# Performance work log

Measured on AMD Instinct MI355X. Metric: run time of the kernel, lower is better.

## Reference

```python
import jax, jax.numpy as jnp
import numpy as np

D_IN = 300      # mol2vec feature dim
H = 64          # neurons[0] == neurons[1]


def _l2norm(x):
    # F.normalize(x, p=2, dim=-1)
    n = jnp.sqrt(jnp.sum(x * x, axis=-1, keepdims=True))
    return x / jnp.maximum(n, 1e-12)


def _scatter_mean(x, row, col, n_nodes):
    # scatter_mean(x[col], row, dim_size=n_nodes); empty rows -> 0
    s = jax.ops.segment_sum(x[col], row, num_segments=n_nodes)
    c = jax.ops.segment_sum(jnp.ones((row.shape[0], 1), x.dtype), row, num_segments=n_nodes)
    return s / jnp.maximum(c, 1.0)


def _sage_base(x, edges, W, b, n_nodes):
    agg = _scatter_mean(x, edges[0], edges[1], n_nodes)
    h = jnp.concatenate([agg, x], axis=1) @ W + b
    return _l2norm(h)


def _sage_deep(x1, x2, pos_e, neg_e, W, b, n_nodes):
    a1 = _scatter_mean(x1, pos_e[0], pos_e[1], n_nodes)
    a2 = _scatter_mean(x2, neg_e[0], neg_e[1], n_nodes)
    h = jnp.concatenate([a1, a2, x1], axis=1) @ W + b
    return _l2norm(h)


def setup_inputs() -> dict:
    key = jax.random.key(0)
    ks = jax.random.split(key, 16)
    N, E = 8192, 262144

    X = jax.random.normal(ks[0], (N, D_IN), dtype=jnp.float32)

    def make_edges(k):
        e = jax.random.randint(k, (2, E), 0, N, dtype=jnp.int64)
        # no self loops (module calls remove_self_loops)
        col = jnp.where(e[1] == e[0], (e[1] + 1) % N, e[1])
        return jnp.stack([e[0], col])

    positive_edges = make_edges(ks[1])
    negative_edges = make_edges(ks[2])

    labels = jax.random.normal(ks[3], (N * N,), dtype=jnp.float32)
    label_mask = jax.random.uniform(ks[4], (N, N), dtype=jnp.float32)

    sd = lambda fan_in: 1.0 / np.sqrt(fan_in)
    W_pos_base = jax.random.normal(ks[5], (2 * D_IN, H), dtype=jnp.float32) * sd(2 * D_IN)
    b_pos_base = jnp.zeros((H,), dtype=jnp.float32)
    W_neg_base = jax.random.normal(ks[6], (2 * D_IN, H), dtype=jnp.float32) * sd(2 * D_IN)
    b_neg_base = jnp.zeros((H,), dtype=jnp.float32)
    W_pos_deep = jax.random.normal(ks[7], (3 * H, H), dtype=jnp.float32) * sd(3 * H)
    b_pos_deep = jnp.zeros((H,), dtype=jnp.float32)
    W_neg_deep = jax.random.normal(ks[8], (3 * H, H), dtype=jnp.float32) * sd(3 * H)
    b_neg_deep = jnp.zeros((H,), dtype=jnp.float32)

    return {
        "X": X, "positive_edges": positive_edges, "negative_edges": negative_edges,
        "labels": labels, "label_mask": label_mask,
        "W_pos_base": W_pos_base, "b_pos_base": b_pos_base,
        "W_neg_base": W_neg_base, "b_neg_base": b_neg_base,
        "W_pos_deep": W_pos_deep, "b_pos_deep": b_pos_deep,
        "W_neg_deep": W_neg_deep, "b_neg_deep": b_neg_deep,
    }


def reference(X, positive_edges, negative_edges, labels, label_mask,
              W_pos_base, b_pos_base, W_neg_base, b_neg_base,
              W_pos_deep, b_pos_deep, W_neg_deep, b_neg_deep):
    N = X.shape[0]
    h_pos = jnp.tanh(_sage_base(X, positive_edges, W_pos_base, b_pos_base, N))
    h_neg = jnp.tanh(_sage_base(X, negative_edges, W_neg_base, b_neg_base, N))
    h_pos2 = jnp.tanh(_sage_deep(h_pos, h_neg, positive_edges, negative_edges, W_pos_deep, b_pos_deep, N))
    h_neg2 = jnp.tanh(_sage_deep(h_neg, h_pos, positive_edges, negative_edges, W_neg_deep, b_neg_deep, N))
    z = jnp.concatenate([h_pos2, h_neg2], axis=1)           # [N, 2H]
    X_mol = _l2norm(z)
    pred = ((X_mol @ X_mol.T) * label_mask).reshape(-1)      # [N*N]
    loss = jnp.mean((pred - labels) ** 2)
    return (loss, X_mol, pred)
```

## Files before the change

### kernel.cpp

```cpp
#include <hip/hip_runtime.h>
#include <hip/hip_bf16.h>

#define DIN 300
#define KP  320
#define NH  64

typedef __bf16 bf16x8 __attribute__((ext_vector_type(8)));
typedef float  f32x4  __attribute__((ext_vector_type(4)));

__device__ inline float wave_sum(float v){
#pragma unroll
  for (int m = 32; m >= 1; m >>= 1) v += __shfl_xor(v, m, 64);
  return v;
}

__global__ __launch_bounds__(256) void k_prep(const float* __restrict__ X,
                                              __hip_bfloat16* __restrict__ Xb,
                                              const float* __restrict__ Wpb,
                                              const float* __restrict__ Wnb,
                                              __hip_bfloat16* __restrict__ Wtb,
                                              const int* __restrict__ pr, const int* __restrict__ nr,
                                              int* __restrict__ cp, int* __restrict__ cn,
                                              int E, int N){
  int b = blockIdx.x;
  if (b < N){
    const float* xr = X + (size_t)b * DIN;
    __hip_bfloat16* o = Xb + (size_t)b * KP;
    for (int k = threadIdx.x; k < KP; k += 256)
      o[k] = __float2bfloat16(k < DIN ? xr[k] : 0.f);
  } else if (b < N + 256){
    int c = b - N;
    int sel = c >> 6, jj = c & 63;
    const float* W = (sel < 2 ? Wpb : Wnb) + (size_t)(sel & 1) * DIN * NH + jj;
    __hip_bfloat16* o = Wtb + (size_t)c * KP;
    for (int k = threadIdx.x; k < KP; k += 256)
      o[k] = __float2bfloat16(k < DIN ? W[(size_t)k * NH] : 0.f);
  } else {
    int i = (b - N - 256) * 256 + threadIdx.x;
    if (i < E){ atomicAdd(cp + pr[i], 1); atomicAdd(cn + nr[i], 1); }
  }
}

__global__ __launch_bounds__(256) void k_gemm_base(const __hip_bfloat16* __restrict__ Xb,
                                                   const __hip_bfloat16* __restrict__ Wtb,
                                                   float* __restrict__ XW){
  const int wave = threadIdx.x >> 6, lane = threadIdx.x & 63;
  const int ti = blockIdx.y * 64 + wave * 16;
  const int cj = blockIdx.x * 64;
  const int r0 = lane & 15, kq = (lane >> 4) * 8;
  const unsigned short* Xp = (const unsigned short*)Xb;
  const unsigned short* Wp = (const unsigned short*)Wtb;
  f32x4 acc[4] = {};
  for (int ks = 0; ks < KP / 32; ++ks){
    int kb = ks * 32 + kq;
    bf16x8 a = *(const bf16x8*)(Xp + (size_t)(ti + r0) * KP + kb);
#pragma unroll
    for (int js = 0; js < 4; ++js){
      bf16x8 b = *(const bf16x8*)(Wp + (size_t)(cj + js * 16 + r0) * KP + kb);
      acc[js] = __builtin_amdgcn_mfma_f32_16x16x32_bf16(a, b, acc[js], 0, 0, 0);
    }
  }
  const int orow = ti + (lane >> 4) * 4;
  const int oc = cj + (lane & 15);
#pragma unroll
  for (int js = 0; js < 4; ++js)
#pragma unroll
    for (int i = 0; i < 4; ++i)
      XW[(size_t)(orow + i) * 256 + oc + js * 16] = acc[js][i];
}

__global__ __launch_bounds__(1024) void k_scan(const int* __restrict__ c0, int* __restrict__ o0,
                                               const int* __restrict__ c1, int* __restrict__ o1, int n){
  const int* cnt = blockIdx.x ? c1 : c0;
  int* off = blockIdx.x ? o1 : o0;
  __shared__ int lds[1024];
  int t = threadIdx.x;
  int ept = n >> 10;
  int s = 0;
  for (int i = 0; i < ept; ++i) s += cnt[t * ept + i];
  lds[t] = s; __syncthreads();
  for (int d = 1; d < 1024; d <<= 1){
    int add = (t >= d) ? lds[t - d] : 0;
    __syncthreads();
    lds[t] += add;
    __syncthreads();
  }
  int base = t ? lds[t - 1] : 0;
  for (int i = 0; i < ept; ++i){ off[t * ept + i] = base; base += cnt[t * ept + i]; }
}

__global__ void k_fill(const int* __restrict__ pr, const int* __restrict__ pc,
                       const int* __restrict__ nr, const int* __restrict__ nc,
                       const int* __restrict__ op, const int* __restrict__ on,
                       int* __restrict__ curp, int* __restrict__ curn,
                       int* __restrict__ adjp, int* __restrict__ adjn, int E){
  int i = blockIdx.x * 256 + threadIdx.x;
  if (i < E){
    int r = pr[i]; int p = atomicAdd(curp + r, 1); adjp[op[r] + p] = pc[i];
    r = nr[i];     p = atomicAdd(curn + r, 1);     adjn[on[r] + p] = nc[i];
  }
}

__device__ inline float gather_mean(const float* __restrict__ XW, const int* __restrict__ adj,
                                    int base, int d, int col){
  float s = 0.f; int j = 0;
  for (; j + 4 <= d; j += 4){
    int n0 = adj[base + j], n1 = adj[base + j + 1], n2 = adj[base + j + 2], n3 = adj[base + j + 3];
    s += XW[(size_t)n0 * 256 + col] + XW[(size_t)n1 * 256 + col]
       + XW[(size_t)n2 * 256 + col] + XW[(size_t)n3 * 256 + col];
  }
  for (; j < d; ++j) s += XW[(size_t)adj[base + j] * 256 + col];
  return s / (float)(d > 0 ? d : 1);
}

__global__ __launch_bounds__(256) void k_base(const float* __restrict__ XW,
    const int* __restrict__ adjp, const int* __restrict__ offp, const int* __restrict__ cntp,
    const int* __restrict__ adjn, const int* __restrict__ offn, const int* __restrict__ cntn,
    const float* __restrict__ bp, const float* __restrict__ bn,
    float* __restrict__ hp, float* __restrict__ hn){
  const int wave = threadIdx.x >> 6, lane = threadIdx.x & 63;
  const int node = blockIdx.x * 4 + wave;
  {
    float s = gather_mean(XW, adjp, offp[node], cntp[node], lane);
    float pre = s + XW[(size_t)node * 256 + 64 + lane] + bp[lane];
    float nrm = sqrtf(wave_sum(pre * pre));
    hp[(size_t)node * 64 + lane] = tanhf(pre / fmaxf(nrm, 1e-12f));
  }
  {
    float s = gather_mean(XW, adjn, offn[node], cntn[node], lane + 128);
    float pre = s + XW[(size_t)node * 256 + 192 + lane] + bn[lane];
    float nrm = sqrtf(wave_sum(pre * pre));
    hn[(size_t)node * 64 + lane] = tanhf(pre / fmaxf(nrm, 1e-12f));
  }
}

__global__ __launch_bounds__(256) void k_deep(const float* __restrict__ hp, const float* __restrict__ hn,
    const int* __restrict__ adjp, const int* __restrict__ offp, const int* __restrict__ cntp,
    const int* __restrict__ adjn, const int* __restrict__ offn, const int* __restrict__ cntn,
    const float* __restrict__ Wpd, const float* __restrict__ bpd,
    const float* __restrict__ Wnd, const float* __restrict__ bnd,
    float* __restrict__ xmol, __hip_bfloat16* __restrict__ Xmb){
  const int wave = threadIdx.x >> 6, lane = threadIdx.x & 63;
  const int node = blockIdx.x * 4 + wave;
  const float mhp = hp[(size_t)node * 64 + lane];
  const float mhn = hn[(size_t)node * 64 + lane];
  float a1p = 0.f, a1n = 0.f;
  {
    int d = cntp[node], base = offp[node]; int j = 0;
    for (; j + 2 <= d; j += 2){
      int n0 = adjp[base + j], n1 = adjp[base + j + 1];
      a1p += hp[(size_t)n0 * 64 + lane] + hp[(size_t)n1 * 64 + lane];
      a1n += hn[(size_t)n0 * 64 + lane] + hn[(size_t)n1 * 64 + lane];
    }
    for (; j < d; ++j){ int n0 = adjp[base + j]; a1p += hp[(size_t)n0 * 64 + lane]; a1n += hn[(size_t)n0 * 64 + lane]; }
    float inv = 1.f / (float)(d > 0 ? d : 1); a1p *= inv; a1n *= inv;
  }
  float a2p = 0.f, a2n = 0.f;
  {
    int d = cntn[node], base = offn[node]; int j = 0;
    for (; j + 2 <= d; j += 2){
      int n0 = adjn[base + j], n1 = adjn[base + j + 1];
      a2p += hn[(size_t)n0 * 64 + lane] + hn[(size_t)n1 * 64 + lane];
      a2n += hp[(size_t)n0 * 64 + lane] + hp[(size_t)n1 * 64 + lane];
    }
    for (; j < d; ++j){ int n0 = adjn[base + j]; a2p += hn[(size_t)n0 * 64 + lane]; a2n += hp[(size_t)n0 * 64 + lane]; }
    float inv = 1.f / (float)(d > 0 ? d : 1); a2p *= inv; a2n *= inv;
  }
  float accp = bpd[lane], accn = bnd[lane];
#pragma unroll 4
  for (int k = 0; k < 64; ++k){
    float p1 = __shfl(a1p, k, 64), p2 = __shfl(a2p, k, 64), p3 = __shfl(mhp, k, 64);
    float q1 = __shfl(a1n, k, 64), q2 = __shfl(a2n, k, 64), q3 = __shfl(mhn, k, 64);
    accp += p1 * Wpd[k * 64 + lane] + p2 * Wpd[(64 + k) * 64 + lane] + p3 * Wpd[(128 + k) * 64 + lane];
    accn += q1 * Wnd[k * 64 + lane] + q2 * Wnd[(64 + k) * 64 + lane] + q3 * Wnd[(128 + k) * 64 + lane];
  }
  float np = sqrtf(wave_sum(accp * accp));
  float h2p = tanhf(accp / fmaxf(np, 1e-12f));
  float nn = sqrtf(wave_sum(accn * accn));
  float h2n = tanhf(accn / fmaxf(nn, 1e-12f));
  float nz = sqrtf(wave_sum(h2p * h2p + h2n * h2n));
  float xp = h2p / fmaxf(nz, 1e-12f);
  float xn = h2n / fmaxf(nz, 1e-12f);
  xmol[(size_t)node * 128 + lane] = xp;
  xmol[(size_t)node * 128 + 64 + lane] = xn;
  Xmb[(size_t)node * 128 + lane] = __float2bfloat16(xp);
  Xmb[(size_t)node * 128 + 64 + lane] = __float2bfloat16(xn);
}

__global__ __launch_bounds__(256, 3) void k_pred(const __hip_bfloat16* __restrict__ Xmb,
    const float* __restrict__ mask, const float* __restrict__ labels,
    float* __restrict__ pred, float* __restrict__ partial, int N){
  const int wave = threadIdx.x >> 6, lane = threadIdx.x & 63;
  const int ti = blockIdx.y * 64 + wave * 16;
  const int tj = blockIdx.x * 128;
  const int r0 = lane & 15, kq = (lane >> 4) * 8;
  const unsigned short* X = (const unsigned short*)Xmb;
  f32x4 acc[2][4] = {};
#pragma unroll
  for (int ks = 0; ks < 4; ++ks){
    int kb = ks * 32 + kq;
    bf16x8 a = *(const bf16x8*)(X + (size_t)(ti + r0) * 128 + kb);
#pragma unroll
    for (int pan = 0; pan < 2; ++pan)
#pragma unroll
      for (int js = 0; js < 4; ++js){
        bf16x8 b = *(const bf16x8*)(X + (size_t)(tj + pan * 64 + js * 16 + r0) * 128 + kb);
        acc[pan][js] = __builtin_amdgcn_mfma_f32_16x16x32_bf16(a, b, acc[pan][js], 0, 0, 0);
      }
  }
  const int hi = lane >> 5, c = lane & 31;
  f32x4 m[8], lb[8];
#pragma unroll
  for (int g = 0; g < 8; ++g){
    size_t idx = (size_t)(ti + g * 2 + hi) * N + tj + c * 4;
    m[g]  = __builtin_nontemporal_load((const f32x4*)(mask + idx));
    lb[g] = __builtin_nontemporal_load((const f32x4*)(labels + idx));
  }
#pragma unroll
  for (int g = 0; g < 8; ++g)
    asm volatile("" : "+v"(m[g]), "+v"(lb[g]));
  __shared__ float tile[4][16][132];
  __shared__ float wsum[4];
  const int rb = (lane >> 4) * 4, c16 = lane & 15;
#pragma unroll
  for (int pan = 0; pan < 2; ++pan)
#pragma unroll
    for (int js = 0; js < 4; ++js)
#pragma unroll
      for (int i = 0; i < 4; ++i)
        tile[wave][rb + i][pan * 64 + js * 16 + c16] = acc[pan][js][i];
  float lsum = 0.f;
#pragma unroll
  for (int g = 0; g < 8; ++g){
    int row = g * 2 + hi;
    f32x4 a = *(const f32x4*)&tile[wave][row][c * 4];
    f32x4 pv = a * m[g];
    f32x4 d = pv - lb[g];
    lsum += d[0]*d[0] + d[1]*d[1] + d[2]*d[2] + d[3]*d[3];
    size_t idx = (size_t)(ti + row) * N + tj + c * 4;
    __builtin_nontemporal_store(pv[0], pred + idx);
    __builtin_nontemporal_store(pv[1], pred + idx + 1);
    __builtin_nontemporal_store(pv[2], pred + idx + 2);
    __builtin_nontemporal_store(pv[3], pred + idx + 3);
  }
  lsum = wave_sum(lsum);
  if (lane == 0) wsum[wave] = lsum;
  __syncthreads();
  if (threadIdx.x == 0)
    partial[blockIdx.y * gridDim.x + blockIdx.x] = wsum[0] + wsum[1] + wsum[2] + wsum[3];
}

__global__ __launch_bounds__(1024) void k_loss_fin(const float* __restrict__ partial,
                                                   float* __restrict__ out, float inv, int n){
  float s = 0.f;
  for (int i = threadIdx.x; i < n; i += 1024) s += partial[i];
  s = wave_sum(s);
  __shared__ float ws[16];
  if ((threadIdx.x & 63) == 0) ws[threadIdx.x >> 6] = s;
  __syncthreads();
  if (threadIdx.x == 0){
    float t = 0.f;
#pragma unroll
    for (int w = 0; w < 16; ++w) t += ws[w];
    out[0] = t * inv;
  }
}

extern "C" void kernel_launch(void* const* d_in, const int* in_sizes, int n_in,
                              void* d_out, int out_size, void* d_ws, size_t ws_size,
                              hipStream_t stream){
  const float* X      = (const float*)d_in[0];
  const int*   pe     = (const int*)d_in[1];
  const int*   ne     = (const int*)d_in[2];
  const float* labels = (const float*)d_in[3];
  const float* mask   = (const float*)d_in[4];
  const float* Wpb    = (const float*)d_in[5];
  const float* bpb    = (const float*)d_in[6];
  const float* Wnb    = (const float*)d_in[7];
  const float* bnb    = (const float*)d_in[8];
  const float* Wpd    = (const float*)d_in[9];
  const float* bpd    = (const float*)d_in[10];
  const float* Wnd    = (const float*)d_in[11];
  const float* bnd    = (const float*)d_in[12];
  const int N = in_sizes[0] / DIN;
  const int E = in_sizes[1] / 2;

  char* ws = (char*)d_ws;
  size_t off = 0;
  auto alloc = [&](size_t bytes){ void* p = ws + off; off = (off + bytes + 255) & ~(size_t)255; return p; };
  float* XW            = (float*)alloc((size_t)N * 256 * 4);
  float* hp            = (float*)alloc((size_t)N * 64 * 4);
  float* hn            = (float*)alloc((size_t)N * 64 * 4);
  __hip_bfloat16* Xmb  = (__hip_bfloat16*)alloc((size_t)N * 128 * 2);
  __hip_bfloat16* Xb   = (__hip_bfloat16*)alloc((size_t)N * KP * 2);
  __hip_bfloat16* Wtb  = (__hip_bfloat16*)alloc((size_t)256 * KP * 2);
  int* adjp            = (int*)alloc((size_t)E * 4);
  int* adjn            = (int*)alloc((size_t)E * 4);
  char* zbase = ws + off;
  int* cntp            = (int*)alloc((size_t)N * 4);
  int* cntn            = (int*)alloc((size_t)N * 4);
  int* curp            = (int*)alloc((size_t)N * 4);
  int* curn            = (int*)alloc((size_t)N * 4);
  size_t zbytes = (size_t)((ws + off) - zbase);
  int* offp            = (int*)alloc((size_t)N * 4);
  int* offn            = (int*)alloc((size_t)N * 4);
  float* partial       = (float*)alloc((size_t)(N / 64) * (N / 128) * 4);
  (void)ws_size; (void)n_in; (void)out_size;

  float* out_loss = (float*)d_out;
  float* out_xmol = out_loss + 1;
  float* out_pred = out_xmol + (size_t)N * 128;

  hipMemsetAsync(zbase, 0, zbytes, stream);
  k_prep<<<N + 256 + (E + 255) / 256, 256, 0, stream>>>(X, Xb, Wpb, Wnb, Wtb,
                                                        pe, ne, cntp, cntn, E, N);
  k_gemm_base<<<dim3(4, N / 64), 256, 0, stream>>>(Xb, Wtb, XW);
  k_scan<<<2, 1024, 0, stream>>>(cntp, offp, cntn, offn, N);
  k_fill<<<(E + 255) / 256, 256, 0, stream>>>(pe, pe + E, ne, ne + E, offp, offn, curp, curn, adjp, adjn, E);
  k_base<<<N / 4, 256, 0, stream>>>(XW, adjp, offp, cntp, adjn, offn, cntn, bpb, bnb, hp, hn);
  k_deep<<<N / 4, 256, 0, stream>>>(hp, hn, adjp, offp, cntp, adjn, offn, cntn,
                                    Wpd, bpd, Wnd, bnd, out_xmol, Xmb);
  k_pred<<<dim3(N / 128, N / 64), 256, 0, stream>>>(Xmb, mask, labels, out_pred, partial, N);
  k_loss_fin<<<1, 1024, 0, stream>>>(partial, out_loss, 1.0f / ((float)N * (float)N), (N / 64) * (N / 128));
}
```

Measured before the change: 367.9 us.

## Vectorize X bf16 conversion, widen gather unrolls, relax k_pred launch bounds

```diff
diff --git a/kernel.cpp b/kernel.cpp
--- a/kernel.cpp
+++ b/kernel.cpp
@@ -7,6 +7,7 @@
 
 typedef __bf16 bf16x8 __attribute__((ext_vector_type(8)));
 typedef float  f32x4  __attribute__((ext_vector_type(4)));
+typedef short  s16x4  __attribute__((ext_vector_type(4)));
 
 __device__ inline float wave_sum(float v){
 #pragma unroll
@@ -25,9 +26,21 @@
   int b = blockIdx.x;
   if (b < N){
     const float* xr = X + (size_t)b * DIN;
-    __hip_bfloat16* o = Xb + (size_t)b * KP;
-    for (int k = threadIdx.x; k < KP; k += 256)
-      o[k] = __float2bfloat16(k < DIN ? xr[k] : 0.f);
+    unsigned short* o = (unsigned short*)(Xb + (size_t)b * KP);
+    int k = threadIdx.x;
+    if (k < 80){
+      s16x4 v;
+      if (k < 75){
+        f32x4 x = *(const f32x4*)(xr + k * 4);
+#pragma unroll
+        for (int j = 0; j < 4; ++j){
+          union { float f; unsigned u; } cv; cv.f = x[j];
+          unsigned r = (cv.u + 0x7FFF + ((cv.u >> 16) & 1)) >> 16;
+          v[j] = (short)r;
+        }
+      } else v = (s16x4){0,0,0,0};
+      *(s16x4*)(o + k * 4) = v;
+    }
   } else if (b < N + 256){
     int c = b - N;
     int sel = c >> 6, jj = c & 63;
@@ -103,13 +116,18 @@
 
 __device__ inline float gather_mean(const float* __restrict__ XW, const int* __restrict__ adj,
                                     int base, int d, int col){
-  float s = 0.f; int j = 0;
-  for (; j + 4 <= d; j += 4){
-    int n0 = adj[base + j], n1 = adj[base + j + 1], n2 = adj[base + j + 2], n3 = adj[base + j + 3];
-    s += XW[(size_t)n0 * 256 + col] + XW[(size_t)n1 * 256 + col]
-       + XW[(size_t)n2 * 256 + col] + XW[(size_t)n3 * 256 + col];
-  }
-  for (; j < d; ++j) s += XW[(size_t)adj[base + j] * 256 + col];
+  float s0 = 0.f, s1 = 0.f, s2 = 0.f, s3 = 0.f;
+  int j = 0;
+  for (; j + 8 <= d; j += 8){
+    int n0 = adj[base + j],     n1 = adj[base + j + 1], n2 = adj[base + j + 2], n3 = adj[base + j + 3];
+    int n4 = adj[base + j + 4], n5 = adj[base + j + 5], n6 = adj[base + j + 6], n7 = adj[base + j + 7];
+    s0 += XW[(size_t)n0 * 256 + col] + XW[(size_t)n4 * 256 + col];
+    s1 += XW[(size_t)n1 * 256 + col] + XW[(size_t)n5 * 256 + col];
+    s2 += XW[(size_t)n2 * 256 + col] + XW[(size_t)n6 * 256 + col];
+    s3 += XW[(size_t)n3 * 256 + col] + XW[(size_t)n7 * 256 + col];
+  }
+  for (; j < d; ++j) s0 += XW[(size_t)adj[base + j] * 256 + col];
+  float s = (s0 + s1) + (s2 + s3);
   return s / (float)(d > 0 ? d : 1);
 }
 
@@ -147,10 +165,13 @@
   float a1p = 0.f, a1n = 0.f;
   {
     int d = cntp[node], base = offp[node]; int j = 0;
-    for (; j + 2 <= d; j += 2){
+    for (; j + 4 <= d; j += 4){
       int n0 = adjp[base + j], n1 = adjp[base + j + 1];
-      a1p += hp[(size_t)n0 * 64 + lane] + hp[(size_t)n1 * 64 + lane];
-      a1n += hn[(size_t)n0 * 64 + lane] + hn[(size_t)n1 * 64 + lane];
+      int n2 = adjp[base + j + 2], n3 = adjp[base + j + 3];
+      a1p += (hp[(size_t)n0 * 64 + lane] + hp[(size_t)n1 * 64 + lane])
+           + (hp[(size_t)n2 * 64 + lane] + hp[(size_t)n3 * 64 + lane]);
+      a1n += (hn[(size_t)n0 * 64 + lane] + hn[(size_t)n1 * 64 + lane])
+           + (hn[(size_t)n2 * 64 + lane] + hn[(size_t)n3 * 64 + lane]);
     }
     for (; j < d; ++j){ int n0 = adjp[base + j]; a1p += hp[(size_t)n0 * 64 + lane]; a1n += hn[(size_t)n0 * 64 + lane]; }
     float inv = 1.f / (float)(d > 0 ? d : 1); a1p *= inv; a1n *= inv;
@@ -158,10 +179,13 @@
   float a2p = 0.f, a2n = 0.f;
   {
     int d = cntn[node], base = offn[node]; int j = 0;
-    for (; j + 2 <= d; j += 2){
+    for (; j + 4 <= d; j += 4){
       int n0 = adjn[base + j], n1 = adjn[base + j + 1];
-      a2p += hn[(size_t)n0 * 64 + lane] + hn[(size_t)n1 * 64 + lane];
-      a2n += hp[(size_t)n0 * 64 + lane] + hp[(size_t)n1 * 64 + lane];
+      int n2 = adjn[base + j + 2], n3 = adjn[base + j + 3];
+      a2p += (hn[(size_t)n0 * 64 + lane] + hn[(size_t)n1 * 64 + lane])
+           + (hn[(size_t)n2 * 64 + lane] + hn[(size_t)n3 * 64 + lane]);
+      a2n += (hp[(size_t)n0 * 64 + lane] + hp[(size_t)n1 * 64 + lane])
+           + (hp[(size_t)n2 * 64 + lane] + hp[(size_t)n3 * 64 + lane]);
     }
     for (; j < d; ++j){ int n0 = adjn[base + j]; a2p += hn[(size_t)n0 * 64 + lane]; a2n += hp[(size_t)n0 * 64 + lane]; }
     float inv = 1.f / (float)(d > 0 ? d : 1); a2p *= inv; a2n *= inv;
@@ -187,7 +211,7 @@
   Xmb[(size_t)node * 128 + 64 + lane] = __float2bfloat16(xn);
 }
 
-__global__ __launch_bounds__(256, 3) void k_pred(const __hip_bfloat16* __restrict__ Xmb,
+__global__ __launch_bounds__(256) void k_pred(const __hip_bfloat16* __restrict__ Xmb,
     const float* __restrict__ mask, const float* __restrict__ labels,
     float* __restrict__ pred, float* __restrict__ partial, int N){
   const int wave = threadIdx.x >> 6, lane = threadIdx.x & 63;
@@ -216,9 +240,6 @@
     m[g]  = __builtin_nontemporal_load((const f32x4*)(mask + idx));
     lb[g] = __builtin_nontemporal_load((const f32x4*)(labels + idx));
   }
-#pragma unroll
-  for (int g = 0; g < 8; ++g)
-    asm volatile("" : "+v"(m[g]), "+v"(lb[g]));
   __shared__ float tile[4][16][132];
   __shared__ float wsum[4];
   const int rb = (lane >> 4) * 4, c16 = lane & 15;
```

Measured after the change: 344.6 us. -6.3%, faster.
